# Optimization experiments

Measured on AMD Instinct MI355X. Metric: run time of the kernel, lower is better.

The kernel has to match this reference:

```python
import jax, jax.numpy as jnp
import numpy as np

# Multi-res hash grid config (tiny-cuda-nn defaults matching input_ch=32 = 16 levels * 2 feats)
L = 16            # n_levels
F = 2             # n_features_per_level
T = 2 ** 19       # hashmap size per level
BASE_RES = 16
FINEST_RES = 512
_b = np.exp((np.log(FINEST_RES) - np.log(BASE_RES)) / (L - 1))
RES = np.floor(BASE_RES * (_b ** np.arange(L))).astype(np.float32)  # (L,)
PRIMES = jnp.array([1, 2654435761, 805459861], dtype=jnp.uint32)
# 8 binary corner offsets of a voxel
CORNERS = jnp.array([[(i >> d) & 1 for d in range(3)] for i in range(8)], dtype=jnp.uint32)  # (8,3)


def hash_encode(x, tables):
    """x: (N,3) in [0,1]; tables: (L, T, F). Returns (N, L*F)."""
    res = jnp.asarray(RES)                              # (L,)
    xs = x[None, :, :] * res[:, None, None]             # (L,N,3) scaled coords
    x0f = jnp.floor(xs)
    frac = xs - x0f                                     # (L,N,3)
    x0 = x0f.astype(jnp.uint32)
    corners = x0[:, :, None, :] + CORNERS[None, None]   # (L,N,8,3) uint32
    # spatial hash: xor of coord*prime, wraparound uint32 mul
    h = (corners[..., 0] * PRIMES[0]) ^ (corners[..., 1] * PRIMES[1]) ^ (corners[..., 2] * PRIMES[2])
    idx = (h % jnp.uint32(T)).astype(jnp.int32)         # (L,N,8)
    gidx = idx + (jnp.arange(L, dtype=jnp.int32) * T)[:, None, None]
    feats = tables.reshape(L * T, F)[gidx]              # (L,N,8,F) gather
    # trilinear weights per corner
    w = jnp.prod(jnp.where(CORNERS[None, None] == 1, frac[:, :, None, :], 1.0 - frac[:, :, None, :]), axis=-1)  # (L,N,8)
    out = jnp.einsum('lnc,lncf->lnf', w, feats)         # (L,N,F)
    return out.transpose(1, 0, 2).reshape(x.shape[0], L * F)


def setup_inputs() -> dict:
    key = jax.random.key(0)
    ks = jax.random.split(key, 16)
    N = 1048576
    W = 128
    pos_flat = jax.random.uniform(ks[0], (N, 3), dtype=jnp.float32)  # world pts in unit cube
    bbox_min = jnp.zeros((3,), dtype=jnp.float32)
    bbox_max = jnp.ones((3,), dtype=jnp.float32)
    tables = jax.random.uniform(ks[1], (L, T, F), dtype=jnp.float32, minval=-1e-4, maxval=1e-4)
    def lin(k, fan_in, fan_out):
        s = 1.0 / np.sqrt(fan_in)
        return jax.random.uniform(k, (fan_in, fan_out), dtype=jnp.float32, minval=-s, maxval=s)
    return {
        'pos_flat': pos_flat, 'bbox_min': bbox_min, 'bbox_max': bbox_max, 'tables': tables,
        'W0': lin(ks[2], L * F, W), 'b0': jnp.zeros((W,), jnp.float32),
        'W1': lin(ks[3], W, W), 'b1': jnp.zeros((W,), jnp.float32),
        'W2': lin(ks[4], W, W), 'b2': jnp.zeros((W,), jnp.float32),
        'W3': lin(ks[5], W, W), 'b3': jnp.zeros((W,), jnp.float32),
        'Wout': lin(ks[6], W, 4), 'bout': jnp.zeros((4,), jnp.float32),
    }


def reference(pos_flat, bbox_min, bbox_max, tables, W0, b0, W1, b1, W2, b2, W3, b3, Wout, bout):
    # normalize into canonical bbox [0,1]^3
    x = (pos_flat - bbox_min) / (bbox_max - bbox_min)
    h = hash_encode(x, tables)                # (N, 32)
    h = jax.nn.relu(h @ W0 + b0)
    h = jax.nn.relu(h @ W1 + b1)
    h = jax.nn.relu(h @ W2 + b2)
    h = jax.nn.relu(h @ W3 + b3)
    raws = h @ Wout + bout                    # (N, 4) rgb + density
    return raws
```

## Files before the change

### kernel.cpp

```cpp
#include <hip/hip_runtime.h>

typedef _Float16 half8 __attribute__((ext_vector_type(8)));
typedef _Float16 half4 __attribute__((ext_vector_type(4)));
typedef _Float16 half2 __attribute__((ext_vector_type(2)));
typedef float    f32x4 __attribute__((ext_vector_type(4)));
typedef float    f32x2 __attribute__((ext_vector_type(2)));
typedef unsigned u32x2 __attribute__((ext_vector_type(2)));
typedef unsigned u32x4 __attribute__((ext_vector_type(4)));

#define TMASK ((1u << 19) - 1u)
#define HSTRIDE 136
constexpr float SCALE = 65536.0f;
constexpr float INV_SCALE = 1.0f / 65536.0f;

__device__ __constant__ unsigned SC_TAB[8]  = {18, 22, 27, 34, 42, 52, 66, 82};
__device__ __constant__ unsigned DOFF_TAB[8] = {0, 5832, 16480, 36163, 75467, 149555, 290163, 577659};
#define DTOTAL 1129027u

__global__ void prep_kernel(const float* __restrict__ W0, const float* __restrict__ W1,
                            const float* __restrict__ W2, const float* __restrict__ W3,
                            const float* __restrict__ Wm,
                            const float* __restrict__ b0, const float* __restrict__ b1,
                            const float* __restrict__ b2, const float* __restrict__ b3,
                            const float* __restrict__ bm,
                            _Float16* __restrict__ wsW, float* __restrict__ wsB,
                            const float* __restrict__ tabSrc, _Float16* __restrict__ tabF,
                            int tabBlocks)
{
    if ((int)blockIdx.x < tabBlocks) {
        size_t i = (size_t)blockIdx.x * 256 + threadIdx.x;
        f32x4 v = ((const f32x4*)tabSrc)[i];
        half4 o;
        o[0] = (_Float16)(v.x * SCALE);
        o[1] = (_Float16)(v.y * SCALE);
        o[2] = (_Float16)(v.z * SCALE);
        o[3] = (_Float16)(v.w * SCALE);
        ((half4*)tabF)[i] = o;
        return;
    }
    int gid = ((int)blockIdx.x - tabBlocks) * 256 + threadIdx.x;
    if (gid < 6912) {
        int tile = gid >> 6, lane = gid & 63;
        const float* W; int K, N, toff;
        if (tile < 8)        { W = W0; K = 32;  N = 128; toff = 0;   }
        else if (tile < 40)  { W = W1; K = 128; N = 128; toff = 8;   }
        else if (tile < 72)  { W = W2; K = 128; N = 128; toff = 40;  }
        else if (tile < 104) { W = W3; K = 128; N = 128; toff = 72;  }
        else                 { W = Wm; K = 128; N = 4;   toff = 104; }
        int tt = tile - toff;
        int KT = K >> 5;
        int nt = tt / KT, kt = tt - nt * KT;
        int n = nt * 16 + (lane & 15);
        int kbase = kt * 32 + (lane >> 4) * 8;
        half8 v;
        #pragma unroll
        for (int j = 0; j < 8; j++) {
            int k = kbase + j;
            float w = (n < N) ? W[k * N + n] : 0.0f;
            v[j] = (_Float16)w;
        }
        *(half8*)(wsW + (size_t)gid * 8) = v;
    } else if (gid < 6912 + 528) {
        int i = gid - 6912;
        float v;
        if (i < 512) {
            int layer = i >> 7, n = i & 127;
            const float* b = (layer == 0) ? b0 : (layer == 1) ? b1 : (layer == 2) ? b2 : b3;
            v = b[n] * SCALE;
        } else {
            int n = i - 512;
            v = (n < 4) ? bm[n] * SCALE : 0.0f;
        }
        wsB[i] = v;
    }
}

__global__ void dense_build(const float* __restrict__ tables, unsigned* __restrict__ dense)
{
    unsigned e = blockIdx.x * 256 + threadIdx.x;
    if (e >= DTOTAL) return;
    int l = 0;
    #pragma unroll
    for (int i = 1; i < 8; i++) l += (e >= DOFF_TAB[i]) ? 1 : 0;
    unsigned local = e - DOFF_TAB[l];
    unsigned s = SC_TAB[l];
    unsigned s2 = s * s;
    unsigned z = local / s2;
    unsigned rem = local - z * s2;
    unsigned y = rem / s;
    unsigned x = rem - y * s;
    unsigned h = (x ^ (y * 2654435761u) ^ (z * 805459861u)) & TMASK;
    const float* src = tables + ((size_t)l * 524288u + h) * 2;
    half2 o; o[0] = (_Float16)(src[0] * SCALE); o[1] = (_Float16)(src[1] * SCALE);
    union { half2 h2; unsigned u; } cv; cv.h2 = o;
    dense[e] = cv.u;
}

__global__ __launch_bounds__(256, 4) void encode_kernel(
    const float* __restrict__ pos, const float* __restrict__ bmn, const float* __restrict__ bmx,
    const _Float16* __restrict__ tabFine, const unsigned* __restrict__ dense,
    _Float16* __restrict__ feat, int npts)
{
    const int lvl0 = (int)(blockIdx.x & 7);
    const int p = (int)(blockIdx.x >> 3) * 256 + (int)threadIdx.x;
    const float bx = bmn[0], by = bmn[1], bz = bmn[2];
    const float nx = (pos[(size_t)p * 3 + 0] - bx) / (bmx[0] - bx);
    const float ny = (pos[(size_t)p * 3 + 1] - by) / (bmx[1] - by);
    const float nz = (pos[(size_t)p * 3 + 2] - bz) / (bmx[2] - bz);
    constexpr float RESL[16] = {16.f, 20.f, 25.f, 32.f, 40.f, 50.f, 64.f, 80.f,
                                101.f, 128.f, 161.f, 203.f, 256.f, 322.f, 406.f, 512.f};
    const int l0 = lvl0, l1 = lvl0 + 8;
    const _Float16* tblB = tabFine + ((size_t)lvl0 << 20);

    unsigned idxBE[4], idxBO[4];
    bool oddB;
    float txB, tyB, tzB;
    {
        const float res = RESL[l1];
        float xs = nx * res, ys = ny * res, zs = nz * res;
        float fx = floorf(xs), fy = floorf(ys), fz = floorf(zs);
        unsigned xi = (unsigned)fx, yi = (unsigned)fy, zi = (unsigned)fz;
        txB = xs - fx; tyB = ys - fy; tzB = zs - fz;
        unsigned hy0 = yi * 2654435761u, hy1 = (yi + 1u) * 2654435761u;
        unsigned hz0 = zi * 805459861u,  hz1 = (zi + 1u) * 805459861u;
        unsigned hyz[4] = {hy0 ^ hz0, hy1 ^ hz0, hy0 ^ hz1, hy1 ^ hz1};
        unsigned e = (xi + 1u) & ~1u;
        unsigned o = xi | 1u;
        oddB = (xi & 1u) != 0u;
        #pragma unroll
        for (int g = 0; g < 4; g++) {
            idxBE[g] = (e ^ hyz[g]) & TMASK;
            idxBO[g] = (o ^ hyz[g]) & TMASK;
        }
    }

    u32x2 sB[4];
    #pragma unroll
    for (int g = 0; g < 4; g++)
        sB[g] = *(const u32x2*)(tblB + (size_t)(idxBE[g] & ~1u) * 2);
    unsigned oBu[4];
    if (oddB) {
        #pragma unroll
        for (int g = 0; g < 4; g++)
            oBu[g] = *(const unsigned*)(tblB + (size_t)idxBO[g] * 2);
    }

    float txA, tyA, tzA;
    unsigned cl[4], ch[4];
    {
        const float res = RESL[l0];
        float xs = nx * res, ys = ny * res, zs = nz * res;
        float fx = floorf(xs), fy = floorf(ys), fz = floorf(zs);
        unsigned xi = (unsigned)fx, yi = (unsigned)fy, zi = (unsigned)fz;
        txA = xs - fx; tyA = ys - fy; tzA = zs - fz;
        const unsigned s = SC_TAB[l0];
        const unsigned s2 = s * s;
        const unsigned* dptr = dense + DOFF_TAB[l0];
        unsigned b00 = xi + s * yi + s2 * zi;
        unsigned bases[4] = {b00, b00 + s, b00 + s2, b00 + s2 + s};
        #pragma unroll
        for (int g = 0; g < 4; g++) {
            cl[g] = dptr[bases[g]];
            ch[g] = dptr[bases[g] + 1];
        }
    }

    float wyzA[4] = {(1.0f - tyA) * (1.0f - tzA), tyA * (1.0f - tzA),
                     (1.0f - tyA) * tzA,          tyA * tzA};
    float wyzB[4] = {(1.0f - tyB) * (1.0f - tzB), tyB * (1.0f - tzB),
                     (1.0f - tyB) * tzB,          tyB * tzB};

    float a0 = 0.0f, a1 = 0.0f;
    #pragma unroll
    for (int g = 0; g < 4; g++) {
        union { unsigned u; half2 h; } lo, hi;
        lo.u = cl[g]; hi.u = ch[g];
        float w0 = wyzA[g] * (1.0f - txA), w1 = wyzA[g] * txA;
        a0 += w0 * (float)lo.h[0] + w1 * (float)hi.h[0];
        a1 += w0 * (float)lo.h[1] + w1 * (float)hi.h[1];
    }
    {
        half2 ov; ov[0] = (_Float16)a0; ov[1] = (_Float16)a1;
        union { half2 h; unsigned u; } cv; cv.h = ov;
        __builtin_nontemporal_store(cv.u, (unsigned*)(feat + ((size_t)l0 * npts + p) * 2));
    }

    float b0 = 0.0f, b1 = 0.0f;
    #pragma unroll
    for (int g = 0; g < 4; g++) {
        union { unsigned u; half2 h; } lo, hi, ov;
        lo.u = sB[g][0]; hi.u = sB[g][1];
        bool pe = (idxBE[g] & 1u) != 0u;
        half2 fe  = pe ? hi.h : lo.h;
        half2 fe1 = pe ? lo.h : hi.h;
        ov.u = oddB ? oBu[g] : 0u;
        half2 fx0 = oddB ? ov.h : fe;
        half2 fx1 = oddB ? fe : fe1;
        float w0 = wyzB[g] * (1.0f - txB), w1 = wyzB[g] * txB;
        b0 += w0 * (float)fx0[0] + w1 * (float)fx1[0];
        b1 += w0 * (float)fx0[1] + w1 * (float)fx1[1];
    }
    {
        half2 ov; ov[0] = (_Float16)b0; ov[1] = (_Float16)b1;
        union { half2 h; unsigned u; } cv; cv.h = ov;
        __builtin_nontemporal_store(cv.u, (unsigned*)(feat + ((size_t)l1 * npts + p) * 2));
    }
}

#define ELANE 68

template<int KT, int TOFF>
__device__ __forceinline__ void layer_fwd4(half8 b[4][4], const half8* __restrict__ wf,
                                           const float* __restrict__ wsB, int li,
                                           unsigned* __restrict__ eb, int lane, int quad,
                                           unsigned srcA, unsigned srcB, int mtbase)
{
    unsigned* wptr = eb + lane * ELANE;
    #pragma unroll
    for (int mt = 0; mt < 8; mt++) {
        f32x4 bias = *(const f32x4*)&wsB[li * 128 + mt * 16 + quad * 4];
        half8 w[KT];
        #pragma unroll
        for (int kt = 0; kt < KT; kt++)
            w[kt] = wf[(size_t)(TOFF + mt * KT + kt) * 64 + lane];
        f32x4 acc[4] = {bias, bias, bias, bias};
        #pragma unroll
        for (int nt = 0; nt < 4; nt++)
            #pragma unroll
            for (int kt = 0; kt < KT; kt++)
                acc[nt] = __builtin_amdgcn_mfma_f32_16x16x32_f16(w[kt], b[nt][kt], acc[nt], 0, 0, 0);
        #pragma unroll
        for (int np = 0; np < 2; np++) {
            union { _Float16 h[8]; u32x4 v; } pk;
            #pragma unroll
            for (int r = 0; r < 4; r++) {
                pk.h[r]     = (_Float16)fmaxf(acc[2 * np][r],     0.0f);
                pk.h[4 + r] = (_Float16)fmaxf(acc[2 * np + 1][r], 0.0f);
            }
            *(u32x4*)(wptr + mt * 8 + np * 4) = pk.v;
        }
    }
    #pragma unroll
    for (int ktp = 0; ktp < 4; ktp++) {
        int mt = 2 * ktp + mtbase;
        u32x4 rA0 = *(const u32x4*)(eb + srcA * ELANE + mt * 8);
        u32x4 rA1 = *(const u32x4*)(eb + srcA * ELANE + mt * 8 + 4);
        u32x4 rB0 = *(const u32x4*)(eb + srcB * ELANE + mt * 8);
        u32x4 rB1 = *(const u32x4*)(eb + srcB * ELANE + mt * 8 + 4);
        union { u32x4 v; half8 h; } c0, c1, c2, c3;
        c0.v = (u32x4){rA0[0], rA0[1], rB0[0], rB0[1]};
        c1.v = (u32x4){rA0[2], rA0[3], rB0[2], rB0[3]};
        c2.v = (u32x4){rA1[0], rA1[1], rB1[0], rB1[1]};
        c3.v = (u32x4){rA1[2], rA1[3], rB1[2], rB1[3]};
        b[0][ktp] = c0.h;
        b[1][ktp] = c1.h;
        b[2][ktp] = c2.h;
        b[3][ktp] = c3.h;
    }
}

__global__ __launch_bounds__(256) void mlp_kernel(
    const unsigned* __restrict__ feat32, const half8* __restrict__ wf,
    const float* __restrict__ wsB, float* __restrict__ out, int npts)
{
    __shared__ __align__(16) unsigned ebuf[4 * 64 * ELANE];
    const int t = threadIdx.x;
    const int lane = t & 63, wv = t >> 6;
    const int col = lane & 15, quad = lane >> 4;
    const long base = (long)blockIdx.x * 256 + wv * 64;
    unsigned* eb = ebuf + wv * (64 * ELANE);
    const int q1 = 2 * (quad & 1);
    const unsigned srcA = (unsigned)(col + 16 * q1);
    const unsigned srcB = (unsigned)(col + 16 * (q1 + 1));
    const int mtbase = quad >> 1;

    half8 b[4][4];
    #pragma unroll
    for (int nt = 0; nt < 4; nt++) {
        const long pt = base + nt * 16 + col;
        union { unsigned u4[4]; half8 v; } cv;
        #pragma unroll
        for (int jj = 0; jj < 4; jj++)
            cv.u4[jj] = feat32[(size_t)(quad * 4 + jj) * npts + pt];
        b[nt][0] = cv.v;
    }

    layer_fwd4<1, 0 >(b, wf, wsB, 0, eb, lane, quad, srcA, srcB, mtbase);
    layer_fwd4<4, 8 >(b, wf, wsB, 1, eb, lane, quad, srcA, srcB, mtbase);
    layer_fwd4<4, 40>(b, wf, wsB, 2, eb, lane, quad, srcA, srcB, mtbase);
    layer_fwd4<4, 72>(b, wf, wsB, 3, eb, lane, quad, srcA, srcB, mtbase);

    f32x4 biaso = *(const f32x4*)&wsB[512 + quad * 4];
    f32x4 acco[4] = {biaso, biaso, biaso, biaso};
    #pragma unroll
    for (int kt = 0; kt < 4; kt++) {
        half8 w = wf[(size_t)(104 + kt) * 64 + lane];
        #pragma unroll
        for (int nt = 0; nt < 4; nt++)
            acco[nt] = __builtin_amdgcn_mfma_f32_16x16x32_f16(w, b[nt][kt], acco[nt], 0, 0, 0);
    }
    if (quad == 0) {
        #pragma unroll
        for (int nt = 0; nt < 4; nt++) {
            f32x4 v;
            #pragma unroll
            for (int r = 0; r < 4; r++) v[r] = acco[nt][r] * INV_SCALE;
            *(f32x4*)(out + (base + nt * 16 + col) * 4) = v;
        }
    }
}

template<int KT, int TOFF, bool RELU>
__device__ __forceinline__ void mlp_layer(_Float16* h, const half8* __restrict__ wf,
                                          const float* __restrict__ wsB, int layerIdx,
                                          int m0, int lane)
{
    const int col = lane & 15, quad = lane >> 4;
    const int sw = (col & 3) << 3;
    half8 a[2][KT];
    #pragma unroll
    for (int mt = 0; mt < 2; mt++)
        #pragma unroll
        for (int kt = 0; kt < KT; kt++)
            a[mt][kt] = *(const half8*)&h[(m0 + mt * 16 + col) * HSTRIDE + ((kt * 32 + quad * 8) ^ sw)];
    f32x4 acc[2][8];
    #pragma unroll
    for (int nt = 0; nt < 8; nt++) {
        float bv = wsB[layerIdx * 128 + nt * 16 + col];
        acc[0][nt] = (f32x4){bv, bv, bv, bv};
        acc[1][nt] = (f32x4){bv, bv, bv, bv};
    }
    #pragma unroll
    for (int nt = 0; nt < 8; nt++) {
        half8 b[KT];
        #pragma unroll
        for (int kt = 0; kt < KT; kt++)
            b[kt] = wf[(size_t)(TOFF + nt * KT + kt) * 64 + lane];
        #pragma unroll
        for (int mt = 0; mt < 2; mt++)
            #pragma unroll
            for (int kt = 0; kt < KT; kt++)
                acc[mt][nt] = __builtin_amdgcn_mfma_f32_16x16x32_f16(a[mt][kt], b[kt], acc[mt][nt], 0, 0, 0);
    }
    #pragma unroll
    for (int mt = 0; mt < 2; mt++)
        #pragma unroll
        for (int nt = 0; nt < 8; nt++) {
            f32x4 v = acc[mt][nt];
            #pragma unroll
            for (int r = 0; r < 4; r++) {
                float x = v[r];
                if (RELU) x = fmaxf(x, 0.0f);
                h[(m0 + mt * 16 + quad * 4 + r) * HSTRIDE + ((nt * 16 + col) ^ (r << 3))] = (_Float16)x;
            }
        }
}

__global__ __launch_bounds__(256, 2) void fused_kernel(
    const float* __restrict__ pos, const float* __restrict__ bmn, const float* __restrict__ bmx,
    const float* __restrict__ tables, const half8* __restrict__ wf, const float* __restrict__ wsB,
    float* __restrict__ out)
{
    __shared__ _Float16 hbuf[128 * HSTRIDE];
    __shared__ float outstage[512];
    const int t = threadIdx.x;
    const long base = (long)blockIdx.x * 128;
    {
        const int p = t >> 1, hh = t & 1;
        const long gp = base + p;
        const float b0x = bmn[0], b0y = bmn[1], b0z = bmn[2];
        const float nx = (pos[gp * 3 + 0] - b0x) / (bmx[0] - b0x);
        const float ny = (pos[gp * 3 + 1] - b0y) / (bmx[1] - b0y);
        const float nz = (pos[gp * 3 + 2] - b0z) / (bmx[2] - b0z);
        constexpr float RLO[8] = {16.f, 20.f, 25.f, 32.f, 40.f, 50.f, 64.f, 80.f};
        constexpr float RHI[8] = {101.f, 128.f, 161.f, 203.f, 256.f, 322.f, 406.f, 512.f};
        half8 fa, fb;
        #pragma unroll
        for (int li = 0; li < 8; li++) {
            const float res = hh ? RHI[li] : RLO[li];
            const float* tbl = tables + ((size_t)(hh * 8 + li) << 20);
            float xs = nx * res, ys = ny * res, zs = nz * res;
            float fx = floorf(xs), fy = floorf(ys), fz = floorf(zs);
            unsigned xi = (unsigned)fx, yi = (unsigned)fy, zi = (unsigned)fz;
            float tx = xs - fx, ty = ys - fy, tz = zs - fz;
            unsigned hx[2] = {xi, xi + 1u};
            unsigned hy[2] = {yi * 2654435761u, (yi + 1u) * 2654435761u};
            unsigned hz[2] = {zi * 805459861u, (zi + 1u) * 805459861u};
            float wx[2] = {1.0f - tx, tx}, wy[2] = {1.0f - ty, ty}, wz[2] = {1.0f - tz, tz};
            float a0 = 0.0f, a1 = 0.0f;
            #pragma unroll
            for (int c = 0; c < 8; c++) {
                unsigned hsh = hx[c & 1] ^ hy[(c >> 1) & 1] ^ hz[c >> 2];
                unsigned idx = hsh & TMASK;
                f32x2 f = *(const f32x2*)(tbl + (size_t)idx * 2);
                float w = wx[c & 1] * wy[(c >> 1) & 1] * wz[c >> 2];
                a0 += w * f.x;
                a1 += w * f.y;
            }
            if (li < 4) { fa[2 * li]       = (_Float16)(a0 * SCALE); fa[2 * li + 1]       = (_Float16)(a1 * SCALE); }
            else        { fb[2 * (li - 4)] = (_Float16)(a0 * SCALE); fb[2 * (li - 4) + 1] = (_Float16)(a1 * SCALE); }
        }
        const int sw = (p & 3) << 3;
        *(half8*)&hbuf[p * HSTRIDE + ((hh * 16) ^ sw)]       = fa;
        *(half8*)&hbuf[p * HSTRIDE + (((hh * 16) + 8) ^ sw)] = fb;
    }
    __syncthreads();
    {
        const int lane = t & 63;
        const int m0 = (t >> 6) * 32;
        mlp_layer<1, 0,   true>(hbuf, wf, wsB, 0, m0, lane);
        mlp_layer<4, 8,   true>(hbuf, wf, wsB, 1, m0, lane);
        mlp_layer<4, 40,  true>(hbuf, wf, wsB, 2, m0, lane);
        mlp_layer<4, 72,  true>(hbuf, wf, wsB, 3, m0, lane);
        const int col = lane & 15, quad = lane >> 4;
        const int sw = (col & 3) << 3;
        half8 a[2][4];
        #pragma unroll
        for (int mt = 0; mt < 2; mt++)
            #pragma unroll
            for (int kt = 0; kt < 4; kt++)
                a[mt][kt] = *(const half8*)&hbuf[(m0 + mt * 16 + col) * HSTRIDE + ((kt * 32 + quad * 8) ^ sw)];
        float bv = wsB[512 + col];
        f32x4 acc[2] = {(f32x4){bv, bv, bv, bv}, (f32x4){bv, bv, bv, bv}};
        #pragma unroll
        for (int kt = 0; kt < 4; kt++) {
            half8 bfr = wf[(size_t)(104 + kt) * 64 + lane];
            #pragma unroll
            for (int mt = 0; mt < 2; mt++)
                acc[mt] = __builtin_amdgcn_mfma_f32_16x16x32_f16(a[mt][kt], bfr, acc[mt], 0, 0, 0);
        }
        if (col < 4) {
            #pragma unroll
            for (int mt = 0; mt < 2; mt++)
                #pragma unroll
                for (int r = 0; r < 4; r++)
                    outstage[(m0 + mt * 16 + quad * 4 + r) * 4 + col] = acc[mt][r] * INV_SCALE;
        }
    }
    __syncthreads();
    if (t < 128) {
        f32x4 v = ((const f32x4*)outstage)[t];
        *(f32x4*)(out + (base + t) * 4) = v;
    }
}

extern "C" void kernel_launch(void* const* d_in, const int* in_sizes, int n_in,
                              void* d_out, int out_size, void* d_ws, size_t ws_size,
                              hipStream_t stream) {
    const float* pos    = (const float*)d_in[0];
    const float* bmn    = (const float*)d_in[1];
    const float* bmx    = (const float*)d_in[2];
    const float* tables = (const float*)d_in[3];
    const float* W0 = (const float*)d_in[4];
    const float* b0 = (const float*)d_in[5];
    const float* W1 = (const float*)d_in[6];
    const float* b1 = (const float*)d_in[7];
    const float* W2 = (const float*)d_in[8];
    const float* b2 = (const float*)d_in[9];
    const float* W3 = (const float*)d_in[10];
    const float* b3 = (const float*)d_in[11];
    const float* Wm = (const float*)d_in[12];
    const float* bm = (const float*)d_in[13];

    const int N = in_sizes[0] / 3;
    const size_t featBytes    = (size_t)N * 16 * 4;
    const size_t tabFineBytes = (size_t)8 * 524288 * 2 * 2;
    const size_t denseBytes   = ((size_t)DTOTAL * 4 + 255) & ~(size_t)255;
    const size_t need = featBytes + tabFineBytes + denseBytes + 110592 + 2112;

    if (ws_size >= need && (N % 256) == 0) {
        _Float16* feat  = (_Float16*)d_ws;
        _Float16* tabF  = (_Float16*)((char*)d_ws + featBytes);
        unsigned* dense = (unsigned*)((char*)d_ws + featBytes + tabFineBytes);
        _Float16* wsW   = (_Float16*)((char*)d_ws + featBytes + tabFineBytes + denseBytes);
        float*    wsB   = (float*)((char*)d_ws + featBytes + tabFineBytes + denseBytes + 110592);
        prep_kernel<<<8192 + 30, 256, 0, stream>>>(W0, W1, W2, W3, Wm, b0, b1, b2, b3, bm,
                                                   wsW, wsB, tables + (size_t)8 * 524288 * 2,
                                                   tabF, 8192);
        dense_build<<<(DTOTAL + 255) / 256, 256, 0, stream>>>(tables, dense);
        encode_kernel<<<(N / 256) * 8, 256, 0, stream>>>(pos, bmn, bmx, tabF, dense, feat, N);
        mlp_kernel<<<N / 256, 256, 0, stream>>>((const unsigned*)feat, (const half8*)wsW,
                                                wsB, (float*)d_out, N);
    } else {
        _Float16* wsW = (_Float16*)d_ws;
        float*    wsB = (float*)((char*)d_ws + 110592);
        prep_kernel<<<30, 256, 0, stream>>>(W0, W1, W2, W3, Wm, b0, b1, b2, b3, bm,
                                            wsW, wsB, tables, (_Float16*)nullptr, 0);
        fused_kernel<<<N / 128, 256, 0, stream>>>(pos, bmn, bmx, tables,
                                                  (const half8*)wsW, wsB, (float*)d_out);
    }
}
```

Measured before the change: 622.1 us.

## Pack dense coarse-level grid into 16-byte x-quads and process two points per thread

The dense lookup table for the eight coarse levels is re-laid out so that each 16-byte slot holds four consecutive x cells, padding x up to a multiple of four. The encoder can then fetch both x-corners with a single 128-bit load, with one extra scalar load only when the cell sits at x mod 4 == 3. Each thread now encodes two points, with all loads for both issued before any interpolation, to keep more gathers in flight. The costs are a slightly larger dense table, more registers per thread, and a fast path that now requires N to be a multiple of 512.

```diff
diff --git a/kernel.cpp b/kernel.cpp
--- a/kernel.cpp
+++ b/kernel.cpp
@@ -13,9 +13,10 @@
 constexpr float SCALE = 65536.0f;
 constexpr float INV_SCALE = 1.0f / 65536.0f;
 
-__device__ __constant__ unsigned SC_TAB[8]  = {18, 22, 27, 34, 42, 52, 66, 82};
-__device__ __constant__ unsigned DOFF_TAB[8] = {0, 5832, 16480, 36163, 75467, 149555, 290163, 577659};
-#define DTOTAL 1129027u
+__device__ __constant__ unsigned SC_TAB[8]   = {18, 22, 27, 34, 42, 52, 66, 82};
+__device__ __constant__ unsigned SX4_TAB[8]  = {5, 6, 7, 9, 11, 13, 17, 21};
+__device__ __constant__ unsigned DOFF16_TAB[8] = {0, 1620, 4524, 9627, 20031, 39435, 74587, 148639};
+#define DSLOT_TOTAL 289843u
 
 __global__ void prep_kernel(const float* __restrict__ W0, const float* __restrict__ W1,
                             const float* __restrict__ W2, const float* __restrict__ W3,
@@ -78,17 +79,19 @@
 __global__ void dense_build(const float* __restrict__ tables, unsigned* __restrict__ dense)
 {
     unsigned e = blockIdx.x * 256 + threadIdx.x;
-    if (e >= DTOTAL) return;
+    if (e >= DSLOT_TOTAL * 4u) return;
+    unsigned slot = e >> 2, j = e & 3u;
     int l = 0;
     #pragma unroll
-    for (int i = 1; i < 8; i++) l += (e >= DOFF_TAB[i]) ? 1 : 0;
-    unsigned local = e - DOFF_TAB[l];
-    unsigned s = SC_TAB[l];
-    unsigned s2 = s * s;
-    unsigned z = local / s2;
-    unsigned rem = local - z * s2;
-    unsigned y = rem / s;
-    unsigned x = rem - y * s;
+    for (int i = 1; i < 8; i++) l += (slot >= DOFF16_TAB[i]) ? 1 : 0;
+    unsigned local = slot - DOFF16_TAB[l];
+    unsigned s = SC_TAB[l], sx4 = SX4_TAB[l];
+    unsigned plane = sx4 * s;
+    unsigned z = local / plane;
+    unsigned rem = local - z * plane;
+    unsigned y = rem / sx4;
+    unsigned xs = rem - y * sx4;
+    unsigned x = xs * 4u + j;
     unsigned h = (x ^ (y * 2654435761u) ^ (z * 805459861u)) & TMASK;
     const float* src = tables + ((size_t)l * 524288u + h) * 2;
     half2 o; o[0] = (_Float16)(src[0] * SCALE); o[1] = (_Float16)(src[1] * SCALE);
@@ -98,112 +101,137 @@
 
 __global__ __launch_bounds__(256, 4) void encode_kernel(
     const float* __restrict__ pos, const float* __restrict__ bmn, const float* __restrict__ bmx,
-    const _Float16* __restrict__ tabFine, const unsigned* __restrict__ dense,
+    const _Float16* __restrict__ tabFine, const u32x4* __restrict__ dense16,
     _Float16* __restrict__ feat, int npts)
 {
     const int lvl0 = (int)(blockIdx.x & 7);
-    const int p = (int)(blockIdx.x >> 3) * 256 + (int)threadIdx.x;
+    const int t = (int)threadIdx.x;
+    const long p0 = (long)(blockIdx.x >> 3) * 512 + t;
     const float bx = bmn[0], by = bmn[1], bz = bmn[2];
-    const float nx = (pos[(size_t)p * 3 + 0] - bx) / (bmx[0] - bx);
-    const float ny = (pos[(size_t)p * 3 + 1] - by) / (bmx[1] - by);
-    const float nz = (pos[(size_t)p * 3 + 2] - bz) / (bmx[2] - bz);
+    const float dxr = bmx[0] - bx, dyr = bmx[1] - by, dzr = bmx[2] - bz;
     constexpr float RESL[16] = {16.f, 20.f, 25.f, 32.f, 40.f, 50.f, 64.f, 80.f,
                                 101.f, 128.f, 161.f, 203.f, 256.f, 322.f, 406.f, 512.f};
-    const int l0 = lvl0, l1 = lvl0 + 8;
+    const int l1 = lvl0 + 8;
     const _Float16* tblB = tabFine + ((size_t)lvl0 << 20);
-
-    unsigned idxBE[4], idxBO[4];
-    bool oddB;
-    float txB, tyB, tzB;
-    {
-        const float res = RESL[l1];
-        float xs = nx * res, ys = ny * res, zs = nz * res;
-        float fx = floorf(xs), fy = floorf(ys), fz = floorf(zs);
-        unsigned xi = (unsigned)fx, yi = (unsigned)fy, zi = (unsigned)fz;
-        txB = xs - fx; tyB = ys - fy; tzB = zs - fz;
-        unsigned hy0 = yi * 2654435761u, hy1 = (yi + 1u) * 2654435761u;
-        unsigned hz0 = zi * 805459861u,  hz1 = (zi + 1u) * 805459861u;
-        unsigned hyz[4] = {hy0 ^ hz0, hy1 ^ hz0, hy0 ^ hz1, hy1 ^ hz1};
-        unsigned e = (xi + 1u) & ~1u;
-        unsigned o = xi | 1u;
-        oddB = (xi & 1u) != 0u;
-        #pragma unroll
-        for (int g = 0; g < 4; g++) {
-            idxBE[g] = (e ^ hyz[g]) & TMASK;
-            idxBO[g] = (o ^ hyz[g]) & TMASK;
-        }
-    }
-
-    u32x2 sB[4];
-    #pragma unroll
-    for (int g = 0; g < 4; g++)
-        sB[g] = *(const u32x2*)(tblB + (size_t)(idxBE[g] & ~1u) * 2);
-    unsigned oBu[4];
-    if (oddB) {
+    const float resF = RESL[l1], resC = RESL[lvl0];
+    const unsigned s   = SC_TAB[lvl0];
+    const unsigned sx4 = SX4_TAB[lvl0];
+    const unsigned plane = sx4 * s;
+    const u32x4* dptr = dense16 + DOFF16_TAB[lvl0];
+
+    unsigned fSlot[2][4], fOdd[2][4], cBase[2][4];
+    unsigned peM[2], kC[2];
+    bool oddF[2], nx3[2];
+    float fF[2][3], fC[2][3];
+
+    #pragma unroll
+    for (int pt = 0; pt < 2; pt++) {
+        const long p = p0 + pt * 256;
+        const float nx = (pos[p * 3 + 0] - bx) / dxr;
+        const float ny = (pos[p * 3 + 1] - by) / dyr;
+        const float nz = (pos[p * 3 + 2] - bz) / dzr;
+        {
+            float xs = nx * resF, ys = ny * resF, zs = nz * resF;
+            float fx = floorf(xs), fy = floorf(ys), fz = floorf(zs);
+            unsigned xi = (unsigned)fx, yi = (unsigned)fy, zi = (unsigned)fz;
+            fF[pt][0] = xs - fx; fF[pt][1] = ys - fy; fF[pt][2] = zs - fz;
+            unsigned hy0 = yi * 2654435761u, hy1 = (yi + 1u) * 2654435761u;
+            unsigned hz0 = zi * 805459861u,  hz1 = (zi + 1u) * 805459861u;
+            unsigned hyz[4] = {hy0 ^ hz0, hy1 ^ hz0, hy0 ^ hz1, hy1 ^ hz1};
+            unsigned e = (xi + 1u) & ~1u, o = xi | 1u;
+            oddF[pt] = (xi & 1u) != 0u;
+            unsigned m = 0;
+            #pragma unroll
+            for (int g = 0; g < 4; g++) {
+                unsigned ie = (e ^ hyz[g]) & TMASK;
+                fSlot[pt][g] = ie & ~1u;
+                m |= (ie & 1u) << g;
+                fOdd[pt][g] = (o ^ hyz[g]) & TMASK;
+            }
+            peM[pt] = m;
+        }
+        {
+            float xs = nx * resC, ys = ny * resC, zs = nz * resC;
+            float fx = floorf(xs), fy = floorf(ys), fz = floorf(zs);
+            unsigned xi = (unsigned)fx, yi = (unsigned)fy, zi = (unsigned)fz;
+            fC[pt][0] = xs - fx; fC[pt][1] = ys - fy; fC[pt][2] = zs - fz;
+            unsigned b00 = (xi >> 2) + sx4 * yi + plane * zi;
+            cBase[pt][0] = b00;
+            cBase[pt][1] = b00 + sx4;
+            cBase[pt][2] = b00 + plane;
+            cBase[pt][3] = b00 + plane + sx4;
+            kC[pt] = xi & 3u;
+            nx3[pt] = (kC[pt] == 3u);
+        }
+    }
+
+    u32x2 fS[2][4]; u32x4 cS[2][4]; unsigned fO[2][4], cN[2][4];
+    #pragma unroll
+    for (int pt = 0; pt < 2; pt++) {
         #pragma unroll
         for (int g = 0; g < 4; g++)
-            oBu[g] = *(const unsigned*)(tblB + (size_t)idxBO[g] * 2);
-    }
-
-    float txA, tyA, tzA;
-    unsigned cl[4], ch[4];
-    {
-        const float res = RESL[l0];
-        float xs = nx * res, ys = ny * res, zs = nz * res;
-        float fx = floorf(xs), fy = floorf(ys), fz = floorf(zs);
-        unsigned xi = (unsigned)fx, yi = (unsigned)fy, zi = (unsigned)fz;
-        txA = xs - fx; tyA = ys - fy; tzA = zs - fz;
-        const unsigned s = SC_TAB[l0];
-        const unsigned s2 = s * s;
-        const unsigned* dptr = dense + DOFF_TAB[l0];
-        unsigned b00 = xi + s * yi + s2 * zi;
-        unsigned bases[4] = {b00, b00 + s, b00 + s2, b00 + s2 + s};
-        #pragma unroll
-        for (int g = 0; g < 4; g++) {
-            cl[g] = dptr[bases[g]];
-            ch[g] = dptr[bases[g] + 1];
-        }
-    }
-
-    float wyzA[4] = {(1.0f - tyA) * (1.0f - tzA), tyA * (1.0f - tzA),
-                     (1.0f - tyA) * tzA,          tyA * tzA};
-    float wyzB[4] = {(1.0f - tyB) * (1.0f - tzB), tyB * (1.0f - tzB),
-                     (1.0f - tyB) * tzB,          tyB * tzB};
-
-    float a0 = 0.0f, a1 = 0.0f;
-    #pragma unroll
-    for (int g = 0; g < 4; g++) {
-        union { unsigned u; half2 h; } lo, hi;
-        lo.u = cl[g]; hi.u = ch[g];
-        float w0 = wyzA[g] * (1.0f - txA), w1 = wyzA[g] * txA;
-        a0 += w0 * (float)lo.h[0] + w1 * (float)hi.h[0];
-        a1 += w0 * (float)lo.h[1] + w1 * (float)hi.h[1];
-    }
-    {
-        half2 ov; ov[0] = (_Float16)a0; ov[1] = (_Float16)a1;
-        union { half2 h; unsigned u; } cv; cv.h = ov;
-        __builtin_nontemporal_store(cv.u, (unsigned*)(feat + ((size_t)l0 * npts + p) * 2));
-    }
-
-    float b0 = 0.0f, b1 = 0.0f;
-    #pragma unroll
-    for (int g = 0; g < 4; g++) {
-        union { unsigned u; half2 h; } lo, hi, ov;
-        lo.u = sB[g][0]; hi.u = sB[g][1];
-        bool pe = (idxBE[g] & 1u) != 0u;
-        half2 fe  = pe ? hi.h : lo.h;
-        half2 fe1 = pe ? lo.h : hi.h;
-        ov.u = oddB ? oBu[g] : 0u;
-        half2 fx0 = oddB ? ov.h : fe;
-        half2 fx1 = oddB ? fe : fe1;
-        float w0 = wyzB[g] * (1.0f - txB), w1 = wyzB[g] * txB;
-        b0 += w0 * (float)fx0[0] + w1 * (float)fx1[0];
-        b1 += w0 * (float)fx0[1] + w1 * (float)fx1[1];
-    }
-    {
-        half2 ov; ov[0] = (_Float16)b0; ov[1] = (_Float16)b1;
-        union { half2 h; unsigned u; } cv; cv.h = ov;
-        __builtin_nontemporal_store(cv.u, (unsigned*)(feat + ((size_t)l1 * npts + p) * 2));
+            fS[pt][g] = *(const u32x2*)(tblB + (size_t)fSlot[pt][g] * 2);
+        #pragma unroll
+        for (int g = 0; g < 4; g++)
+            cS[pt][g] = dptr[cBase[pt][g]];
+        if (oddF[pt]) {
+            #pragma unroll
+            for (int g = 0; g < 4; g++)
+                fO[pt][g] = *(const unsigned*)(tblB + (size_t)fOdd[pt][g] * 2);
+        }
+        if (nx3[pt]) {
+            #pragma unroll
+            for (int g = 0; g < 4; g++)
+                cN[pt][g] = *(const unsigned*)(dptr + cBase[pt][g] + 1);
+        }
+    }
+
+    #pragma unroll
+    for (int pt = 0; pt < 2; pt++) {
+        const long p = p0 + pt * 256;
+        {
+            float tx = fF[pt][0], ty = fF[pt][1], tz = fF[pt][2];
+            float wyz[4] = {(1.0f - ty) * (1.0f - tz), ty * (1.0f - tz),
+                            (1.0f - ty) * tz,          ty * tz};
+            float b0 = 0.0f, b1 = 0.0f;
+            #pragma unroll
+            for (int g = 0; g < 4; g++) {
+                union { unsigned u; half2 h; } lo, hi, ov;
+                lo.u = fS[pt][g][0]; hi.u = fS[pt][g][1];
+                bool pe = ((peM[pt] >> g) & 1u) != 0u;
+                half2 fe  = pe ? hi.h : lo.h;
+                half2 fe1 = pe ? lo.h : hi.h;
+                ov.u = oddF[pt] ? fO[pt][g] : 0u;
+                half2 fx0 = oddF[pt] ? ov.h : fe;
+                half2 fx1 = oddF[pt] ? fe : fe1;
+                float w0 = wyz[g] * (1.0f - tx), w1 = wyz[g] * tx;
+                b0 += w0 * (float)fx0[0] + w1 * (float)fx1[0];
+                b1 += w0 * (float)fx0[1] + w1 * (float)fx1[1];
+            }
+            half2 ov2; ov2[0] = (_Float16)b0; ov2[1] = (_Float16)b1;
+            union { half2 h; unsigned u; } cv; cv.h = ov2;
+            __builtin_nontemporal_store(cv.u, (unsigned*)(feat + ((size_t)l1 * npts + p) * 2));
+        }
+        {
+            float tx = fC[pt][0], ty = fC[pt][1], tz = fC[pt][2];
+            float wyz[4] = {(1.0f - ty) * (1.0f - tz), ty * (1.0f - tz),
+                            (1.0f - ty) * tz,          ty * tz};
+            unsigned k = kC[pt];
+            unsigned kp1 = (k < 3u) ? (k + 1u) : 0u;
+            float a0 = 0.0f, a1 = 0.0f;
+            #pragma unroll
+            for (int g = 0; g < 4; g++) {
+                union { unsigned u; half2 h; } u0, u1;
+                u0.u = cS[pt][g][k];
+                u1.u = nx3[pt] ? cN[pt][g] : cS[pt][g][kp1];
+                float w0 = wyz[g] * (1.0f - tx), w1 = wyz[g] * tx;
+                a0 += w0 * (float)u0.h[0] + w1 * (float)u1.h[0];
+                a1 += w0 * (float)u0.h[1] + w1 * (float)u1.h[1];
+            }
+            half2 ov2; ov2[0] = (_Float16)a0; ov2[1] = (_Float16)a1;
+            union { half2 h; unsigned u; } cv; cv.h = ov2;
+            __builtin_nontemporal_store(cv.u, (unsigned*)(feat + ((size_t)lvl0 * npts + p) * 2));
+        }
     }
 }
 
@@ -465,10 +493,10 @@
     const int N = in_sizes[0] / 3;
     const size_t featBytes    = (size_t)N * 16 * 4;
     const size_t tabFineBytes = (size_t)8 * 524288 * 2 * 2;
-    const size_t denseBytes   = ((size_t)DTOTAL * 4 + 255) & ~(size_t)255;
+    const size_t denseBytes   = ((size_t)DSLOT_TOTAL * 16 + 255) & ~(size_t)255;
     const size_t need = featBytes + tabFineBytes + denseBytes + 110592 + 2112;
 
-    if (ws_size >= need && (N % 256) == 0) {
+    if (ws_size >= need && (N % 512) == 0) {
         _Float16* feat  = (_Float16*)d_ws;
         _Float16* tabF  = (_Float16*)((char*)d_ws + featBytes);
         unsigned* dense = (unsigned*)((char*)d_ws + featBytes + tabFineBytes);
@@ -477,8 +505,9 @@
         prep_kernel<<<8192 + 30, 256, 0, stream>>>(W0, W1, W2, W3, Wm, b0, b1, b2, b3, bm,
                                                    wsW, wsB, tables + (size_t)8 * 524288 * 2,
                                                    tabF, 8192);
-        dense_build<<<(DTOTAL + 255) / 256, 256, 0, stream>>>(tables, dense);
-        encode_kernel<<<(N / 256) * 8, 256, 0, stream>>>(pos, bmn, bmx, tabF, dense, feat, N);
+        dense_build<<<(DSLOT_TOTAL * 4 + 255) / 256, 256, 0, stream>>>(tables, dense);
+        encode_kernel<<<(N / 512) * 8, 256, 0, stream>>>(pos, bmn, bmx, tabF,
+                                                         (const u32x4*)dense, feat, N);
         mlp_kernel<<<N / 256, 256, 0, stream>>>((const unsigned*)feat, (const half8*)wsW,
                                                 wsB, (float*)d_out, N);
     } else {
```

New measurement: 615.6 us. About the same (-1.0%).
